# Kernel tuning notes

Measured on AMD Instinct MI355X. Metric: run time of the kernel, lower is better.

## Reference

```python
import jax, jax.numpy as jnp
import numpy as np

B, L, D, H = 2, 2048, 1024, 16
HD = D // H
KW = 4  # conv kernel width


def layernorm(x, g, b, eps=1e-5):
    m = jnp.mean(x, axis=-1, keepdims=True)
    v = jnp.var(x, axis=-1, keepdims=True)
    return (x - m) / jnp.sqrt(v + eps) * g + b


def causal_conv(x, w, b):
    # torch Conv1d(k=4, padding=3, groups=D) then truncate to L => causal depthwise conv
    # out[t] = sum_j w[:, j] * x[t - 3 + j] + b
    xp = jnp.pad(x, ((0, 0), (KW - 1, 0), (0, 0)))
    Lx = x.shape[1]
    out = b
    for j in range(KW):
        out = out + xp[:, j:j + Lx, :] * w[:, j]
    return out


def setup_inputs() -> dict:
    key = jax.random.key(0)
    ks = jax.random.split(key, 16)
    r = lambda i, shape, s=0.02: jax.random.normal(ks[i], shape, jnp.float32) * s
    return dict(
        x=r(0, (B, L, D), 1.0),
        Wqkv=r(1, (D, 3 * D)), Wout=r(2, (D, D)),
        Wgate=r(3, (D, D)), bgate=jnp.zeros((D,), jnp.float32),
        fn_g=jnp.ones((D,), jnp.float32), fn_b=jnp.zeros((D,), jnp.float32),
        dn_g=jnp.ones((D,), jnp.float32), dn_b=jnp.zeros((D,), jnp.float32),
        dWq=r(4, (D, D)), dWk=r(5, (D, D)), dWv=r(6, (D, D)), dWo=r(7, (D, D)),
        Wbeta=r(8, (D, H)), bbeta=jnp.zeros((H,), jnp.float32),
        cq_w=r(9, (D, KW), 0.1), cq_b=jnp.zeros((D,), jnp.float32),
        ck_w=r(10, (D, KW), 0.1), ck_b=jnp.zeros((D,), jnp.float32),
        ln_g=jnp.ones((D,), jnp.float32), ln_b=jnp.zeros((D,), jnp.float32),
    )


def _delta_scan(q, k, v, beta):
    # q,k,v: (B,L,H,HD) ; beta: (B,L,H)
    Bx = q.shape[0]
    S0 = jnp.zeros((Bx, H, HD, HD), q.dtype)
    z0 = jnp.zeros((Bx, H, HD), q.dtype)

    def step(carry, inp):
        S, z = carry
        q_t, k_t, v_t, b_t = inp  # (B,H,HD) x3, (B,H)
        y = jnp.einsum('bhij,bhj->bhi', S, q_t)
        denom = jnp.einsum('bhi,bhi->bh', z, q_t)[..., None] + 1e-6
        y = y / denom
        old = jnp.einsum('bhij,bhj->bhi', S, k_t)
        delta = v_t - old
        S = S + b_t[..., None, None] * jnp.einsum('bhi,bhj->bhij', delta, k_t)
        z = z + b_t[..., None] * k_t
        return (S, z), y

    xs = (jnp.moveaxis(q, 1, 0), jnp.moveaxis(k, 1, 0),
          jnp.moveaxis(v, 1, 0), jnp.moveaxis(beta, 1, 0))
    (S, z), ys = jax.lax.scan(step, (S0, z0), xs)
    return jnp.moveaxis(ys, 0, 1), S, z  # (B,L,H,HD)


def _forward(x, Wqkv, Wout, Wgate, bgate, fn_g, fn_b, dn_g, dn_b,
             dWq, dWk, dWv, dWo, Wbeta, bbeta, cq_w, cq_b, ck_w, ck_b, ln_g, ln_b):
    Bx, Lx, Dx = x.shape
    # ---- flash (full causal, L<=2048 branch) ----
    qkv = (x @ Wqkv).reshape(Bx, Lx, 3, H, HD)
    q = jnp.moveaxis(qkv[:, :, 0], 1, 2)  # (B,H,L,HD)
    k = jnp.moveaxis(qkv[:, :, 1], 1, 2)
    v = jnp.moveaxis(qkv[:, :, 2], 1, 2)
    scale = HD ** -0.5
    scores = jnp.einsum('bhqd,bhkd->bhqk', q, k) * scale
    causal = jnp.tril(jnp.ones((Lx, Lx), bool))
    scores = jnp.where(causal, scores, -jnp.inf)
    attn = jax.nn.softmax(scores, axis=-1)
    flash = jnp.einsum('bhqk,bhkd->bhqd', attn, v)
    flash = jnp.moveaxis(flash, 1, 2).reshape(Bx, Lx, Dx) @ Wout
    flash = layernorm(flash, fn_g, fn_b)
    # ---- delta branch ----
    dq = causal_conv(x @ dWq, cq_w, cq_b).reshape(Bx, Lx, H, HD)
    dk = causal_conv(x @ dWk, ck_w, ck_b).reshape(Bx, Lx, H, HD)
    dv = (x @ dWv).reshape(Bx, Lx, H, HD)
    dk = dk / jnp.maximum(jnp.linalg.norm(dk, axis=-1, keepdims=True), 1e-12)
    beta = jax.nn.sigmoid(x @ Wbeta + bbeta)  # (B,L,H)
    ys, S, z = _delta_scan(dq, dk, dv, beta)
    delta_out = layernorm(ys.reshape(Bx, Lx, Dx) @ dWo, ln_g, ln_b)  # DeltaAttention layer_norm
    delta_out = layernorm(delta_out, dn_g, dn_b)  # hybrid delta_norm
    # ---- gate ----
    gate = jax.nn.sigmoid(x @ Wgate + bgate)
    out = gate * flash + (1.0 - gate) * delta_out
    return out, S, z


def reference(x, Wqkv, Wout, Wgate, bgate, fn_g, fn_b, dn_g, dn_b,
              dWq, dWk, dWv, dWo, Wbeta, bbeta, cq_w, cq_b, ck_w, ck_b, ln_g, ln_b):
    return _forward(x, Wqkv, Wout, Wgate, bgate, fn_g, fn_b, dn_g, dn_b,
                    dWq, dWk, dWv, dWo, Wbeta, bbeta, cq_w, cq_b, ck_w, ck_b, ln_g, ln_b)
```

## Files before the change

kernel.cpp:

```cpp
#include <hip/hip_runtime.h>
#include <hip/hip_bf16.h>

constexpr int B_ = 2, L_ = 2048, D_ = 1024, H_ = 16;

using bf16x8 = __attribute__((ext_vector_type(8))) short;
using f32x4  = __attribute__((ext_vector_type(4))) float;

__device__ __forceinline__ short f2b(float f) {
  union { float f; unsigned int u; } v; v.f = f;
  unsigned int r = (v.u + 0x7FFFu + ((v.u >> 16) & 1u)) >> 16;
  return (short)r;
}
__device__ __forceinline__ float b2f(unsigned short h) {
  union { unsigned int u; float f; } v; v.u = ((unsigned int)h) << 16; return v.f;
}
__device__ __forceinline__ void split2(float x, float y, unsigned int& h, unsigned int& l) {
  unsigned short hx = (unsigned short)f2b(x), hy = (unsigned short)f2b(y);
  h = (unsigned int)hx | ((unsigned int)hy << 16);
  unsigned short lx = (unsigned short)f2b(x - b2f(hx)), ly = (unsigned short)f2b(y - b2f(hy));
  l = (unsigned int)lx | ((unsigned int)ly << 16);
}
__device__ __forceinline__ float dot4(float4 a, float4 b) {
  return a.x * b.x + a.y * b.y + a.z * b.z + a.w * b.w;
}

__global__ __launch_bounds__(256) void tcast(const float* __restrict__ W, short* __restrict__ Wt,
                                             int N, int K) {
  __shared__ float T[64][65];
  int n0 = blockIdx.x * 64, k0 = blockIdx.y * 64;
  int tid = threadIdx.x;
#pragma unroll
  for (int i = 0; i < 16; ++i) {
    int idx = i * 256 + tid;
    int r = idx >> 6, c = idx & 63;
    T[r][c] = W[(size_t)(k0 + r) * N + n0 + c];
  }
  __syncthreads();
#pragma unroll
  for (int i = 0; i < 16; ++i) {
    int idx = i * 256 + tid;
    int rr = idx >> 6, cc = idx & 63;
    Wt[(size_t)(n0 + rr) * K + k0 + cc] = f2b(T[cc][rr]);
  }
}

__global__ __launch_bounds__(256) void tcast2(const float* __restrict__ W1, const float* __restrict__ W2,
                                              short* __restrict__ Wt1, short* __restrict__ Wt2) {
  __shared__ float T[64][65];
  const float* W = blockIdx.z ? W2 : W1;
  short* Wt = blockIdx.z ? Wt2 : Wt1;
  int n0 = blockIdx.x * 64, k0 = blockIdx.y * 64;
  int tid = threadIdx.x;
#pragma unroll
  for (int i = 0; i < 16; ++i) {
    int idx = i * 256 + tid;
    int r = idx >> 6, c = idx & 63;
    T[r][c] = W[(size_t)(k0 + r) * 1024 + n0 + c];
  }
  __syncthreads();
#pragma unroll
  for (int i = 0; i < 16; ++i) {
    int idx = i * 256 + tid;
    int rr = idx >> 6, cc = idx & 63;
    Wt[(size_t)(n0 + rr) * 1024 + k0 + cc] = f2b(T[cc][rr]);
  }
}

__global__ __launch_bounds__(256) void tcast_split2(const float* __restrict__ W1, const float* __restrict__ W2,
                                                    short* __restrict__ Wh1, short* __restrict__ Wl1,
                                                    short* __restrict__ Wh2, short* __restrict__ Wl2) {
  __shared__ float T[64][65];
  const float* W = blockIdx.z ? W2 : W1;
  short* Wh = blockIdx.z ? Wh2 : Wh1;
  short* Wl = blockIdx.z ? Wl2 : Wl1;
  int n0 = blockIdx.x * 64, k0 = blockIdx.y * 64;
  int tid = threadIdx.x;
#pragma unroll
  for (int i = 0; i < 16; ++i) {
    int idx = i * 256 + tid;
    int r = idx >> 6, c = idx & 63;
    T[r][c] = W[(size_t)(k0 + r) * 1024 + n0 + c];
  }
  __syncthreads();
#pragma unroll
  for (int i = 0; i < 16; ++i) {
    int idx = i * 256 + tid;
    int rr = idx >> 6, cc = idx & 63;
    float w = T[cc][rr];
    short h = f2b(w);
    short l = f2b(w - b2f((unsigned short)h));
    size_t o = (size_t)(n0 + rr) * 1024 + k0 + cc;
    Wh[o] = h;
    Wl[o] = l;
  }
}

template <int BN, typename CT>
__device__ __forceinline__ void gemm_bt_body(const float* __restrict__ A, const short* __restrict__ Wt,
                                             CT* __restrict__ C, int N, int K, int bx, int by) {
  constexpr int MT = (BN == 128) ? 4 : 2;
  constexpr int NT = 4;
  __shared__ __align__(16) short As[128 * 32];
  __shared__ __align__(16) short Bs[BN * 32];
  int tid = threadIdx.x;
  int wave = tid >> 6, lane = tid & 63, quad = lane >> 4, l15 = lane & 15;
  int m0 = by * 128, n0 = bx * BN;
  int wm = (BN == 128) ? (wave >> 1) * 64 : wave * 32;
  int wn = (BN == 128) ? (wave & 1) * 64 : 0;
  f32x4 acc[MT][NT];
#pragma unroll
  for (int mt = 0; mt < MT; ++mt)
#pragma unroll
    for (int nt = 0; nt < NT; ++nt) acc[mt][nt] = (f32x4){0.f, 0.f, 0.f, 0.f};

  for (int k0 = 0; k0 < K; k0 += 32) {
    __syncthreads();
#pragma unroll
    for (int i = 0; i < 2; ++i) {
      int chunk = i * 256 + tid;
      int m = chunk >> 2, kc = (chunk & 3) * 8;
      const float* ap = A + (size_t)(m0 + m) * K + k0 + kc;
      float4 a0 = *(const float4*)ap;
      float4 a1 = *(const float4*)(ap + 4);
      __hip_bfloat162 c0 = __float22bfloat162_rn(make_float2(a0.x, a0.y));
      __hip_bfloat162 c1 = __float22bfloat162_rn(make_float2(a0.z, a0.w));
      __hip_bfloat162 c2 = __float22bfloat162_rn(make_float2(a1.x, a1.y));
      __hip_bfloat162 c3 = __float22bfloat162_rn(make_float2(a1.z, a1.w));
      uint4 u;
      u.x = *(unsigned int*)&c0; u.y = *(unsigned int*)&c1;
      u.z = *(unsigned int*)&c2; u.w = *(unsigned int*)&c3;
      *(uint4*)&As[m * 32 + kc] = u;
    }
#pragma unroll
    for (int i = 0; i < BN * 4 / 256; ++i) {
      int chunk = i * 256 + tid;
      int n = chunk >> 2, kc = (chunk & 3) * 8;
      uint4 w = *(const uint4*)(Wt + (size_t)(n0 + n) * K + k0 + kc);
      *(uint4*)&Bs[n * 32 + kc] = w;
    }
    __syncthreads();
    bf16x8 af[MT], bf[NT];
#pragma unroll
    for (int mt = 0; mt < MT; ++mt) af[mt] = *(bf16x8*)&As[(wm + mt * 16 + l15) * 32 + quad * 8];
#pragma unroll
    for (int nt = 0; nt < NT; ++nt) bf[nt] = *(bf16x8*)&Bs[(wn + nt * 16 + l15) * 32 + quad * 8];
#pragma unroll
    for (int mt = 0; mt < MT; ++mt)
#pragma unroll
      for (int nt = 0; nt < NT; ++nt)
        acc[mt][nt] = __builtin_amdgcn_mfma_f32_16x16x32_bf16(af[mt], bf[nt], acc[mt][nt], 0, 0, 0);
  }
#pragma unroll
  for (int mt = 0; mt < MT; ++mt)
#pragma unroll
    for (int nt = 0; nt < NT; ++nt)
#pragma unroll
      for (int r = 0; r < 4; ++r) {
        size_t idx = (size_t)(m0 + wm + mt * 16 + quad * 4 + r) * N + n0 + wn + nt * 16 + l15;
        if constexpr (sizeof(CT) == 2) C[idx] = f2b(acc[mt][nt][r]);
        else C[idx] = acc[mt][nt][r];
      }
}

__global__ __launch_bounds__(256) void gemm_bt_h(const float* __restrict__ A, const short* __restrict__ Wt,
                                                 short* __restrict__ C, int N, int K) {
  gemm_bt_body<128, short>(A, Wt, C, N, K, blockIdx.x, blockIdx.y);
}

__global__ __launch_bounds__(256) void gemm_bt2(const float* __restrict__ A, const short* __restrict__ Wt1,
                                                const short* __restrict__ Wt2, float* __restrict__ C1,
                                                float* __restrict__ C2) {
  gemm_bt_body<64, float>(A, blockIdx.z ? Wt2 : Wt1, blockIdx.z ? C2 : C1, 1024, 1024,
                          blockIdx.x, blockIdx.y);
}

__global__ __launch_bounds__(256) void gemm_bt2_hA(const short* __restrict__ A1, const short* __restrict__ Wt1,
                                                   const short* __restrict__ A2, const short* __restrict__ Wt2,
                                                   float* __restrict__ C1, float* __restrict__ C2) {
  constexpr int K = 1024, N = 1024;
  const short* A = blockIdx.z ? A2 : A1;
  const short* Wt = blockIdx.z ? Wt2 : Wt1;
  float* C = blockIdx.z ? C2 : C1;
  __shared__ __align__(16) short As[128 * 32];
  __shared__ __align__(16) short Bs[64 * 32];
  int tid = threadIdx.x;
  int wave = tid >> 6, lane = tid & 63, quad = lane >> 4, l15 = lane & 15;
  int m0 = blockIdx.y * 128, n0 = blockIdx.x * 64;
  int wm = wave * 32;
  f32x4 acc[2][4];
#pragma unroll
  for (int mt = 0; mt < 2; ++mt)
#pragma unroll
    for (int nt = 0; nt < 4; ++nt) acc[mt][nt] = (f32x4){0.f, 0.f, 0.f, 0.f};
  for (int k0 = 0; k0 < K; k0 += 32) {
    __syncthreads();
#pragma unroll
    for (int i = 0; i < 2; ++i) {
      int chunk = i * 256 + tid;
      int m = chunk >> 2, kc = (chunk & 3) * 8;
      *(uint4*)&As[m * 32 + kc] = *(const uint4*)(A + (size_t)(m0 + m) * K + k0 + kc);
    }
    {
      int n = tid >> 2, kc = (tid & 3) * 8;
      *(uint4*)&Bs[n * 32 + kc] = *(const uint4*)(Wt + (size_t)(n0 + n) * K + k0 + kc);
    }
    __syncthreads();
    bf16x8 af[2], bf[4];
#pragma unroll
    for (int mt = 0; mt < 2; ++mt) af[mt] = *(bf16x8*)&As[(wm + mt * 16 + l15) * 32 + quad * 8];
#pragma unroll
    for (int nt = 0; nt < 4; ++nt) bf[nt] = *(bf16x8*)&Bs[(nt * 16 + l15) * 32 + quad * 8];
#pragma unroll
    for (int mt = 0; mt < 2; ++mt)
#pragma unroll
      for (int nt = 0; nt < 4; ++nt)
        acc[mt][nt] = __builtin_amdgcn_mfma_f32_16x16x32_bf16(af[mt], bf[nt], acc[mt][nt], 0, 0, 0);
  }
#pragma unroll
  for (int mt = 0; mt < 2; ++mt)
#pragma unroll
    for (int nt = 0; nt < 4; ++nt)
#pragma unroll
      for (int r = 0; r < 4; ++r) {
        size_t idx = (size_t)(m0 + wm + mt * 16 + quad * 4 + r) * N + n0 + nt * 16 + l15;
        C[idx] = acc[mt][nt][r];
      }
}

__global__ __launch_bounds__(256) void gemm_bt_split2(const float* __restrict__ A,
                                                      const short* __restrict__ Wh1, const short* __restrict__ Wl1,
                                                      const short* __restrict__ Wh2, const short* __restrict__ Wl2,
                                                      float* __restrict__ C1, float* __restrict__ C2) {
  constexpr int K = 1024, N = 1024;
  const short* Wh = blockIdx.z ? Wh2 : Wh1;
  const short* Wl = blockIdx.z ? Wl2 : Wl1;
  float* C = blockIdx.z ? C2 : C1;
  __shared__ __align__(16) short Ash[128 * 32];
  __shared__ __align__(16) short Asl[128 * 32];
  __shared__ __align__(16) short Bsh[64 * 32];
  __shared__ __align__(16) short Bsl[64 * 32];
  int tid = threadIdx.x;
  int wave = tid >> 6, lane = tid & 63, quad = lane >> 4, l15 = lane & 15;
  int m0 = blockIdx.y * 128, n0 = blockIdx.x * 64;
  int wm = wave * 32;
  f32x4 acc[2][4];
#pragma unroll
  for (int mt = 0; mt < 2; ++mt)
#pragma unroll
    for (int nt = 0; nt < 4; ++nt) acc[mt][nt] = (f32x4){0.f, 0.f, 0.f, 0.f};

  for (int k0 = 0; k0 < K; k0 += 32) {
    __syncthreads();
#pragma unroll
    for (int i = 0; i < 2; ++i) {
      int chunk = i * 256 + tid;
      int m = chunk >> 2, kc = (chunk & 3) * 8;
      const float* ap = A + (size_t)(m0 + m) * K + k0 + kc;
      float4 a0 = *(const float4*)ap;
      float4 a1 = *(const float4*)(ap + 4);
      uint4 uh, ul;
      split2(a0.x, a0.y, uh.x, ul.x);
      split2(a0.z, a0.w, uh.y, ul.y);
      split2(a1.x, a1.y, uh.z, ul.z);
      split2(a1.z, a1.w, uh.w, ul.w);
      *(uint4*)&Ash[m * 32 + kc] = uh;
      *(uint4*)&Asl[m * 32 + kc] = ul;
    }
    {
      int n = tid >> 2, kc = (tid & 3) * 8;
      size_t off = (size_t)(n0 + n) * K + k0 + kc;
      *(uint4*)&Bsh[n * 32 + kc] = *(const uint4*)(Wh + off);
      *(uint4*)&Bsl[n * 32 + kc] = *(const uint4*)(Wl + off);
    }
    __syncthreads();
    bf16x8 ah[2], al[2], bh[4], bl[4];
#pragma unroll
    for (int mt = 0; mt < 2; ++mt) {
      ah[mt] = *(bf16x8*)&Ash[(wm + mt * 16 + l15) * 32 + quad * 8];
      al[mt] = *(bf16x8*)&Asl[(wm + mt * 16 + l15) * 32 + quad * 8];
    }
#pragma unroll
    for (int nt = 0; nt < 4; ++nt) {
      bh[nt] = *(bf16x8*)&Bsh[(nt * 16 + l15) * 32 + quad * 8];
      bl[nt] = *(bf16x8*)&Bsl[(nt * 16 + l15) * 32 + quad * 8];
    }
#pragma unroll
    for (int mt = 0; mt < 2; ++mt)
#pragma unroll
      for (int nt = 0; nt < 4; ++nt) {
        f32x4 a = acc[mt][nt];
        a = __builtin_amdgcn_mfma_f32_16x16x32_bf16(al[mt], bh[nt], a, 0, 0, 0);
        a = __builtin_amdgcn_mfma_f32_16x16x32_bf16(ah[mt], bl[nt], a, 0, 0, 0);
        a = __builtin_amdgcn_mfma_f32_16x16x32_bf16(ah[mt], bh[nt], a, 0, 0, 0);
        acc[mt][nt] = a;
      }
  }
#pragma unroll
  for (int mt = 0; mt < 2; ++mt)
#pragma unroll
    for (int nt = 0; nt < 4; ++nt)
#pragma unroll
      for (int r = 0; r < 4; ++r) {
        size_t idx = (size_t)(m0 + wm + mt * 16 + quad * 4 + r) * N + n0 + nt * 16 + l15;
        C[idx] = acc[mt][nt][r];
      }
}

struct DeltaSmem {
  float MKl[2][32 * 68];
  float BqMl[2][32 * 36];
  float Vl[2][32 * 5];
  float bll[2][32];
  float dnl[2][32];
  float zil[2][64];
  float S0l[4 * 68];
  float Y0l[32 * 5];
  float Rtl[4 * 36];
  float z0l[64];
  float qzl[32];
};
struct AttnSmem {
  short Kl[64 * 64];
  short Vt[64 * 64];
  short Pl[64 * 64];
};

__device__ __forceinline__ void delta_body(char* smraw, int bidx,
                                           const float* __restrict__ dq, const float* __restrict__ dk,
                                           const float* __restrict__ dv, const float* __restrict__ beta,
                                           const float* __restrict__ MK_g, const float* __restrict__ BqM_g,
                                           const float* __restrict__ denB_g, const float* __restrict__ zinc_g,
                                           short* __restrict__ ys_h, float* __restrict__ outS,
                                           float* __restrict__ outZ) {
  DeltaSmem& sm = *reinterpret_cast<DeltaSmem*>(smraw);
  int bh = bidx & 31, grp = bidx >> 5;
  int b = bh >> 4, h = bh & 15;
  int i0 = grp * 4;
  int tid = threadIdx.x;
  int r = tid >> 3, j8 = (tid & 7) * 8;
  int js = tid & 7;
  size_t kqbase = (size_t)(b * L_) * 1024 + h * 64;

  for (int e = tid; e < 4 * 68; e += 256) sm.S0l[e] = 0.f;
  if (tid < 64) sm.z0l[tid] = 0.f;

  float4 kAc, kBc, qAc, qBc, kAn, kBn, qAn, qBn;
  float4 mA, mB, bqA, bqB;
  bqA = bqB = make_float4(0.f, 0.f, 0.f, 0.f);
  float vr = 0.f, blr = 0.f, dnb = 0.f, zi = 0.f;

#define KQLOAD(CN, KA, KB, QA, QB) { \
    size_t rb_ = kqbase + (size_t)((CN) * 32 + r) * 1024 + j8; \
    KA = ((const float4*)(dk + rb_))[0]; KB = ((const float4*)(dk + rb_))[1]; \
    QA = ((const float4*)(dq + rb_))[0]; QB = ((const float4*)(dq + rb_))[1]; \
  }
#define AUXLOAD(CN) { \
    size_t cb_ = (size_t)(bh * 64 + (CN)); \
    const float* mkp_ = MK_g + (cb_ * 32 + r) * 64 + j8; \
    mA = ((const float4*)mkp_)[0]; mB = ((const float4*)mkp_)[1]; \
    if (tid < 128) { \
      const float* bqp_ = BqM_g + cb_ * 1024 + (tid >> 2) * 32 + (tid & 3) * 8; \
      bqA = ((const float4*)bqp_)[0]; bqB = ((const float4*)bqp_)[1]; \
      vr = dv[(size_t)(b * L_ + (CN) * 32 + (tid >> 2)) * 1024 + h * 64 + i0 + (tid & 3)]; \
    } \
    if (tid < 32) { blr = beta[(size_t)(b * L_ + (CN) * 32 + tid) * 16 + h]; dnb = denB_g[cb_ * 32 + tid]; } \
    if (tid < 64) zi = zinc_g[cb_ * 64 + tid]; \
  }
#define AUXSTORE(NX) { \
    *(float4*)&sm.MKl[NX][r * 68 + j8] = mA; *(float4*)&sm.MKl[NX][r * 68 + j8 + 4] = mB; \
    if (tid < 128) { \
      int t_ = tid >> 2, s8_ = (tid & 3) * 8; \
      *(float4*)&sm.BqMl[NX][t_ * 36 + s8_] = bqA; \
      *(float4*)&sm.BqMl[NX][t_ * 36 + s8_ + 4] = bqB; \
      sm.Vl[NX][t_ * 5 + (tid & 3)] = vr; \
    } \
    if (tid < 32) { sm.bll[NX][tid] = blr; sm.dnl[NX][tid] = dnb; } \
    if (tid < 64) sm.zil[NX][tid] = zi; \
  }

  KQLOAD(0, kAc, kBc, qAc, qBc);
  AUXLOAD(0);
  AUXSTORE(0);
  __syncthreads();

  for (int c = 0; c < 64; ++c) {
    int cur = c & 1, nxt = cur ^ 1;
    int cn = (c + 1 < 64) ? c + 1 : 63;
    KQLOAD(cn, kAn, kBn, qAn, qBn);
    AUXLOAD(cn);
    {
      float aK[4], aY[4];
#pragma unroll
      for (int i = 0; i < 4; ++i) {
        float4 s0 = *(float4*)&sm.S0l[i * 68 + j8];
        float4 s1 = *(float4*)&sm.S0l[i * 68 + j8 + 4];
        aK[i] = dot4(kAc, s0) + dot4(kBc, s1);
        aY[i] = dot4(qAc, s0) + dot4(qBc, s1);
      }
      float4 z0 = *(float4*)&sm.z0l[j8];
      float4 z1 = *(float4*)&sm.z0l[j8 + 4];
      float aZ = dot4(qAc, z0) + dot4(qBc, z1);
#pragma unroll
      for (int off = 1; off <= 4; off <<= 1) {
#pragma unroll
        for (int i = 0; i < 4; ++i) {
          aK[i] += __shfl_xor(aK[i], off);
          aY[i] += __shfl_xor(aY[i], off);
        }
        aZ += __shfl_xor(aZ, off);
      }
      if (js == 0) {
        float be = sm.bll[cur][r];
#pragma unroll
        for (int i = 0; i < 4; ++i) {
          sm.Rtl[i * 36 + r] = be * (sm.Vl[cur][r * 5 + i] - aK[i]);
          sm.Y0l[r * 5 + i] = aY[i];
        }
        sm.qzl[r] = aZ;
      }
    }
    __syncthreads();
    if (tid < 128) {
      int i2 = tid >> 5;
      int j2 = (tid & 31) * 2;
      float a0 = sm.S0l[i2 * 68 + j2];
      float a1 = sm.S0l[i2 * 68 + j2 + 1];
#pragma unroll
      for (int s4i = 0; s4i < 8; ++s4i) {
        float4 rt = *(float4*)&sm.Rtl[i2 * 36 + s4i * 4];
        float2 m0 = *(float2*)&sm.MKl[cur][(s4i * 4 + 0) * 68 + j2];
        float2 m1 = *(float2*)&sm.MKl[cur][(s4i * 4 + 1) * 68 + j2];
        float2 m2 = *(float2*)&sm.MKl[cur][(s4i * 4 + 2) * 68 + j2];
        float2 m3 = *(float2*)&sm.MKl[cur][(s4i * 4 + 3) * 68 + j2];
        a0 += rt.x * m0.x + rt.y * m1.x + rt.z * m2.x + rt.w * m3.x;
        a1 += rt.x * m0.y + rt.y * m1.y + rt.z * m2.y + rt.w * m3.y;
      }
      sm.S0l[i2 * 68 + j2] = a0;
      sm.S0l[i2 * 68 + j2 + 1] = a1;
      if (tid < 64) sm.z0l[tid] += sm.zil[cur][tid];
    } else {
      int t = (tid >> 2) & 31;
      int i = tid & 3;
      float acc = sm.Y0l[t * 5 + i];
#pragma unroll
      for (int s4i = 0; s4i < 8; ++s4i)
        acc += dot4(*(float4*)&sm.BqMl[cur][t * 36 + s4i * 4], *(float4*)&sm.Rtl[i * 36 + s4i * 4]);
      float y = acc / (sm.qzl[t] + sm.dnl[cur][t] + 1e-6f);
      ys_h[(size_t)(b * L_ + c * 32 + t) * 1024 + h * 64 + i0 + i] = f2b(y);
    }
    AUXSTORE(nxt);
    kAc = kAn; kBc = kBn; qAc = qAn; qBc = qBn;
    __syncthreads();
  }
#undef KQLOAD
#undef AUXLOAD
#undef AUXSTORE
  {
    int i = tid >> 6, j = tid & 63;
    outS[((size_t)(bh * 64) + i0 + i) * 64 + j] = sm.S0l[i * 68 + j];
  }
  if (grp == 0 && tid < 64) outZ[bh * 64 + tid] = sm.z0l[tid];
}

__device__ __forceinline__ void attn_body(char* smraw, int idx, const short* __restrict__ qkv,
                                          short* __restrict__ outp_h) {
  AttnSmem& sm = *reinterpret_cast<AttnSmem*>(smraw);
  int qb = 31 - (idx & 31), h = (idx >> 5) & 15, b = idx >> 9;
  int tid = threadIdx.x;
  int wave = tid >> 6, lane = tid & 63;
  int quad = lane >> 4, l15 = lane & 15;
  int qrow = qb * 64 + wave * 16 + l15;
  bf16x8 qf[2];
  {
    const short* qbase = qkv + (size_t)(b * L_ + qrow) * 3072 + h * 64;
#pragma unroll
    for (int s = 0; s < 2; ++s) qf[s] = *(const bf16x8*)(qbase + s * 32 + quad * 8);
  }
  f32x4 Of[4];
  float mrow[4], lrow[4], alpha[4];
#pragma unroll
  for (int dt = 0; dt < 4; ++dt) Of[dt] = (f32x4){0.f, 0.f, 0.f, 0.f};
#pragma unroll
  for (int r = 0; r < 4; ++r) { mrow[r] = -1e30f; lrow[r] = 0.f; }

  for (int kt = 0; kt <= qb; ++kt) {
    __syncthreads();
#pragma unroll
    for (int it = 0; it < 2; ++it) {
      int e8 = tid + it * 256;
      int key = e8 >> 3, g = e8 & 7;
      const short* src = qkv + ((size_t)((b * L_ + kt * 64 + key) * 3) + 1) * 1024 + h * 64 + g * 8;
      *(bf16x8*)&sm.Kl[key * 64 + ((g ^ (key & 7)) << 3)] = *(const bf16x8*)src;
    }
    {
      int key4 = tid >> 4;
      int d4 = tid & 15;
      const short* vsrc = qkv + ((size_t)((b * L_ + kt * 64 + key4 * 4) * 3) + 2) * 1024 + h * 64 + d4 * 4;
      short4 v0 = *(const short4*)vsrc;
      short4 v1 = *(const short4*)(vsrc + 3072);
      short4 v2 = *(const short4*)(vsrc + 6144);
      short4 v3 = *(const short4*)(vsrc + 9216);
      short vr0[4] = {v0.x, v0.y, v0.z, v0.w};
      short vr1[4] = {v1.x, v1.y, v1.z, v1.w};
      short vr2[4] = {v2.x, v2.y, v2.z, v2.w};
      short vr3[4] = {v3.x, v3.y, v3.z, v3.w};
      int kg = key4 >> 1, k7b = (key4 & 1) * 4;
#pragma unroll
      for (int jj = 0; jj < 4; ++jj) {
        int d = d4 * 4 + jj;
        short4 sv;
        sv.x = vr0[jj]; sv.y = vr1[jj]; sv.z = vr2[jj]; sv.w = vr3[jj];
        *(short4*)&sm.Vt[d * 64 + ((kg ^ (d & 7)) << 3) + k7b] = sv;
      }
    }
    __syncthreads();
    f32x4 sc[4];
#pragma unroll
    for (int nt = 0; nt < 4; ++nt) sc[nt] = (f32x4){0.f, 0.f, 0.f, 0.f};
#pragma unroll
    for (int s = 0; s < 2; ++s) {
#pragma unroll
      for (int nt = 0; nt < 4; ++nt) {
        int key = nt * 16 + l15;
        bf16x8 kf = *(bf16x8*)&sm.Kl[key * 64 + (((4 * s + quad) ^ (key & 7)) << 3)];
        sc[nt] = __builtin_amdgcn_mfma_f32_16x16x32_bf16(qf[s], kf, sc[nt], 0, 0, 0);
      }
    }
    bool diag = (kt == qb);
#pragma unroll
    for (int r = 0; r < 4; ++r) {
      float sv[4];
#pragma unroll
      for (int nt = 0; nt < 4; ++nt) {
        float v = sc[nt][r] * 0.125f;
        if (diag && (nt * 16 + l15 > wave * 16 + quad * 4 + r)) v = -1e30f;
        sv[nt] = v;
      }
      float mx = fmaxf(fmaxf(sv[0], sv[1]), fmaxf(sv[2], sv[3]));
      mx = fmaxf(mx, __shfl_xor(mx, 1));
      mx = fmaxf(mx, __shfl_xor(mx, 2));
      mx = fmaxf(mx, __shfl_xor(mx, 4));
      mx = fmaxf(mx, __shfl_xor(mx, 8));
      float mnew = fmaxf(mrow[r], mx);
      float al = __expf(mrow[r] - mnew);
      mrow[r] = mnew;
      alpha[r] = al;
      int prow = wave * 16 + quad * 4 + r;
      int r7 = prow & 7;
      float ps = 0.f;
#pragma unroll
      for (int nt = 0; nt < 4; ++nt) {
        float p = __expf(sv[nt] - mnew);
        ps += p;
        sm.Pl[prow * 64 + ((((nt << 1) + (l15 >> 3)) ^ r7) << 3) + (l15 & 7)] = f2b(p);
      }
      ps += __shfl_xor(ps, 1);
      ps += __shfl_xor(ps, 2);
      ps += __shfl_xor(ps, 4);
      ps += __shfl_xor(ps, 8);
      lrow[r] = lrow[r] * al + ps;
    }
#pragma unroll
    for (int dt = 0; dt < 4; ++dt)
#pragma unroll
      for (int r = 0; r < 4; ++r) Of[dt][r] *= alpha[r];
#pragma unroll
    for (int s = 0; s < 2; ++s) {
      bf16x8 pf = *(bf16x8*)&sm.Pl[(wave * 16 + l15) * 64 + (((4 * s + quad) ^ (l15 & 7)) << 3)];
#pragma unroll
      for (int dt = 0; dt < 4; ++dt) {
        int d = dt * 16 + l15;
        bf16x8 vf = *(bf16x8*)&sm.Vt[d * 64 + (((4 * s + quad) ^ (d & 7)) << 3)];
        Of[dt] = __builtin_amdgcn_mfma_f32_16x16x32_bf16(pf, vf, Of[dt], 0, 0, 0);
      }
    }
  }
#pragma unroll
  for (int r = 0; r < 4; ++r) alpha[r] = 1.f / lrow[r];
  int orow = qb * 64 + wave * 16 + quad * 4;
#pragma unroll
  for (int dt = 0; dt < 4; ++dt)
#pragma unroll
    for (int r = 0; r < 4; ++r)
      outp_h[(size_t)(b * L_ + orow + r) * 1024 + h * 64 + dt * 16 + l15] = f2b(Of[dt][r] * alpha[r]);
}

__global__ __launch_bounds__(256) void attn_delta_fused(
    const short* __restrict__ qkv, short* __restrict__ attnO_h,
    const float* __restrict__ dq, const float* __restrict__ dk,
    const float* __restrict__ dv, const float* __restrict__ beta,
    const float* __restrict__ MK_g, const float* __restrict__ BqM_g,
    const float* __restrict__ denB_g, const float* __restrict__ zinc_g,
    short* __restrict__ ys_h, float* __restrict__ outS, float* __restrict__ outZ) {
  __shared__ __align__(16) char smem[sizeof(DeltaSmem)];
  static_assert(sizeof(DeltaSmem) >= sizeof(AttnSmem), "overlay");
  if (blockIdx.x < 512)
    delta_body(smem, blockIdx.x, dq, dk, dv, beta, MK_g, BqM_g, denB_g, zinc_g, ys_h, outS, outZ);
  else
    attn_body(smem, blockIdx.x - 512, qkv, attnO_h);
}

__global__ __launch_bounds__(256) void ln2mix_f(const float* __restrict__ X,
                                                const float* __restrict__ g1, const float* __restrict__ b1,
                                                const float* __restrict__ g2, const float* __restrict__ b2,
                                                const float* __restrict__ gpre, const float* __restrict__ bgate,
                                                const float* __restrict__ foraw,
                                                const float* __restrict__ fng, const float* __restrict__ fnb,
                                                float* __restrict__ outp) {
  int row = blockIdx.x, tid = threadIdx.x;
  const float* xr = X + (size_t)row * D_;
  const float* fr = foraw + (size_t)row * D_;
  __shared__ float rs[4], rss[4], frs[4], frss[4];
  float v[4], f[4];
  float s = 0.f, ss = 0.f, fs = 0.f, fss = 0.f;
#pragma unroll
  for (int i = 0; i < 4; ++i) {
    v[i] = xr[tid + i * 256]; s += v[i]; ss += v[i] * v[i];
    f[i] = fr[tid + i * 256]; fs += f[i]; fss += f[i] * f[i];
  }
#pragma unroll
  for (int off = 32; off; off >>= 1) {
    s += __shfl_xor(s, off); ss += __shfl_xor(ss, off);
    fs += __shfl_xor(fs, off); fss += __shfl_xor(fss, off);
  }
  if ((tid & 63) == 0) { rs[tid >> 6] = s; rss[tid >> 6] = ss; frs[tid >> 6] = fs; frss[tid >> 6] = fss; }
  __syncthreads();
  float S = rs[0] + rs[1] + rs[2] + rs[3];
  float SS = rss[0] + rss[1] + rss[2] + rss[3];
  float FS = frs[0] + frs[1] + frs[2] + frs[3];
  float FSS = frss[0] + frss[1] + frss[2] + frss[3];
  float mean = S * (1.f / 1024.f);
  float var = SS * (1.f / 1024.f) - mean * mean;
  float inv = rsqrtf(var + 1e-5f);
  float fmean = FS * (1.f / 1024.f);
  float fvar = FSS * (1.f / 1024.f) - fmean * fmean;
  float finv = rsqrtf(fvar + 1e-5f);
  s = 0.f; ss = 0.f;
#pragma unroll
  for (int i = 0; i < 4; ++i) {
    int c = tid + i * 256;
    v[i] = (v[i] - mean) * inv * g1[c] + b1[c];
    s += v[i]; ss += v[i] * v[i];
  }
#pragma unroll
  for (int off = 32; off; off >>= 1) { s += __shfl_xor(s, off); ss += __shfl_xor(ss, off); }
  __syncthreads();
  if ((tid & 63) == 0) { rs[tid >> 6] = s; rss[tid >> 6] = ss; }
  __syncthreads();
  S = rs[0] + rs[1] + rs[2] + rs[3];
  SS = rss[0] + rss[1] + rss[2] + rss[3];
  mean = S * (1.f / 1024.f);
  var = SS * (1.f / 1024.f) - mean * mean;
  inv = rsqrtf(var + 1e-5f);
#pragma unroll
  for (int i = 0; i < 4; ++i) {
    int c = tid + i * 256;
    size_t idx = (size_t)row * D_ + c;
    float w = (v[i] - mean) * inv * g2[c] + b2[c];
    float fl = (f[i] - fmean) * finv * fng[c] + fnb[c];
    float gg = 1.f / (1.f + __expf(-(gpre[idx] + bgate[c])));
    outp[idx] = gg * fl + (1.f - gg) * w;
  }
}

__global__ __launch_bounds__(256) void convnorm_kernel(const float* __restrict__ qin, const float* __restrict__ kin,
                                                       const float* __restrict__ qw, const float* __restrict__ qb,
                                                       const float* __restrict__ kw, const float* __restrict__ kb,
                                                       float* __restrict__ qout, float* __restrict__ kout) {
  int path = blockIdx.y;
  int row = blockIdx.x * 4 + (threadIdx.x >> 6);
  int lane = threadIdx.x & 63;
  int bl = row >> 4, h = row & 15;
  int t = bl & (L_ - 1);
  int d = h * 64 + lane;
  size_t idx = (size_t)bl * D_ + d;
  const float* xin = path ? kin : qin;
  const float* w = path ? kw : qw;
  const float* bias = path ? kb : qb;
  float acc = bias[d];
#pragma unroll
  for (int j = 0; j < 4; ++j) {
    int tt = t - 3 + j;
    if (tt >= 0) acc += w[d * 4 + j] * xin[idx + (size_t)(j - 3) * D_];
  }
  if (path) {
    float n2 = acc * acc;
#pragma unroll
    for (int off = 32; off; off >>= 1) n2 += __shfl_xor(n2, off);
    acc = acc / fmaxf(sqrtf(n2), 1e-12f);
    kout[idx] = acc;
  } else {
    qout[idx] = acc;
  }
}

__global__ __launch_bounds__(256) void beta_kernel(const float* __restrict__ xf, const float* __restrict__ Wb,
                                                   const float* __restrict__ bb, float* __restrict__ beta) {
  int row = blockIdx.x, tid = threadIdx.x;
  int h = tid & 15, seg = tid >> 4;
  const float* xr = xf + (size_t)row * D_ + seg * 64;
  const float* wp = Wb + (seg * 64) * H_ + h;
  float p = 0.f;
  for (int k = 0; k < 64; ++k) p += xr[k] * wp[k * H_];
  __shared__ float red[16][17];
  red[seg][h] = p;
  __syncthreads();
  if (tid < 16) {
    float s = bb[tid];
#pragma unroll
    for (int s2 = 0; s2 < 16; ++s2) s += red[s2][tid];
    beta[(size_t)row * H_ + tid] = 1.f / (1.f + __expf(-s));
  }
}

__global__ __launch_bounds__(256) void prep_kernel(const float* __restrict__ dq, const float* __restrict__ dk,
                                                   const float* __restrict__ beta,
                                                   float* __restrict__ MK_g, float* __restrict__ BqM_g,
                                                   float* __restrict__ denB_g, float* __restrict__ zinc_g) {
  __shared__ __align__(16) float Kl[32 * 68];
  __shared__ __align__(16) float Ql[32 * 68];
  __shared__ __align__(16) float Ml[32 * 36];
  __shared__ __align__(16) float Xl[32 * 36];
  __shared__ __align__(16) float Bql[32 * 36];
  __shared__ __align__(16) float bl[32];
  int c = blockIdx.x, bh = blockIdx.y;
  int b = bh >> 4, h = bh & 15;
  int t0 = c * 32;
  int tid = threadIdx.x;
#pragma unroll
  for (int rep = 0; rep < 2; ++rep) {
    int id = tid * 2 + rep;
    int r = id >> 4, j4 = id & 15;
    size_t gi = (size_t)(b * L_ + t0 + r) * 1024 + h * 64 + j4 * 4;
    *(float4*)&Kl[r * 68 + j4 * 4] = *(const float4*)&dk[gi];
    *(float4*)&Ql[r * 68 + j4 * 4] = *(const float4*)&dq[gi];
  }
  if (tid < 32) bl[tid] = beta[(size_t)(b * L_ + t0 + tid) * 16 + h];
  __syncthreads();
  int t = tid >> 3, s0 = (tid & 7) * 4;
  float accA[4] = {0.f, 0.f, 0.f, 0.f}, accB[4] = {0.f, 0.f, 0.f, 0.f};
#pragma unroll
  for (int k4 = 0; k4 < 16; ++k4) {
    float4 kt = *(float4*)&Kl[t * 68 + k4 * 4];
    float4 qt = *(float4*)&Ql[t * 68 + k4 * 4];
#pragma unroll
    for (int j = 0; j < 4; ++j) {
      float4 ks = *(float4*)&Kl[(s0 + j) * 68 + k4 * 4];
      accA[j] += dot4(kt, ks);
      accB[j] += dot4(qt, ks);
    }
  }
#pragma unroll
  for (int j = 0; j < 4; ++j) {
    int s = s0 + j;
    Ml[t * 36 + s] = (s < t) ? bl[t] * accA[j] : ((s == t) ? 1.f : 0.f);
    Bql[t * 36 + s] = (s < t) ? accB[j] : 0.f;
  }
  __syncthreads();
  if (tid < 32) {
    int col = tid;
    float xr[32];
#pragma unroll
    for (int tt = 0; tt < 32; ++tt) {
      float x = (tt == col) ? 1.f : 0.f;
#pragma unroll
      for (int s = 0; s < tt; ++s) x -= Ml[tt * 36 + s] * xr[s];
      xr[tt] = x;
      Xl[tt * 36 + col] = x;
    }
  }
  __syncthreads();
  size_t cb = (size_t)(bh * 64 + c);
  {
    int s = tid >> 3, j8 = (tid & 7) * 8;
    float4 m0 = make_float4(0.f, 0.f, 0.f, 0.f);
    float4 m1 = make_float4(0.f, 0.f, 0.f, 0.f);
#pragma unroll
    for (int t2 = 0; t2 < 32; ++t2) {
      float xv = Xl[t2 * 36 + s];
      float4 k0 = *(float4*)&Kl[t2 * 68 + j8];
      float4 k1 = *(float4*)&Kl[t2 * 68 + j8 + 4];
      m0.x += xv * k0.x; m0.y += xv * k0.y; m0.z += xv * k0.z; m0.w += xv * k0.w;
      m1.x += xv * k1.x; m1.y += xv * k1.y; m1.z += xv * k1.z; m1.w += xv * k1.w;
    }
    float* mkp = MK_g + (cb * 32 + s) * 64 + j8;
    *(float4*)mkp = m0;
    *(float4*)(mkp + 4) = m1;
  }
  {
    int tt = tid >> 3, s4 = (tid & 7) * 4;
    float4 acc = make_float4(0.f, 0.f, 0.f, 0.f);
#pragma unroll
    for (int u4 = 0; u4 < 8; ++u4) {
      float4 bq = *(float4*)&Bql[tt * 36 + u4 * 4];
      float4 x0 = *(float4*)&Xl[(u4 * 4 + 0) * 36 + s4];
      float4 x1 = *(float4*)&Xl[(u4 * 4 + 1) * 36 + s4];
      float4 x2 = *(float4*)&Xl[(u4 * 4 + 2) * 36 + s4];
      float4 x3 = *(float4*)&Xl[(u4 * 4 + 3) * 36 + s4];
      acc.x += bq.x * x0.x + bq.y * x1.x + bq.z * x2.x + bq.w * x3.x;
      acc.y += bq.x * x0.y + bq.y * x1.y + bq.z * x2.y + bq.w * x3.y;
      acc.z += bq.x * x0.z + bq.y * x1.z + bq.z * x2.z + bq.w * x3.z;
      acc.w += bq.x * x0.w + bq.y * x1.w + bq.z * x2.w + bq.w * x3.w;
    }
    *(float4*)&BqM_g[cb * 1024 + tt * 32 + s4] = acc;
  }
  if (tid < 32) {
    float a = 0.f;
#pragma unroll
    for (int s4i = 0; s4i < 8; ++s4i)
      a += dot4(*(float4*)&Bql[tid * 36 + s4i * 4], *(float4*)&bl[s4i * 4]);
    denB_g[cb * 32 + tid] = a;
  }
  if (tid >= 64 && tid < 128) {
    int j = tid - 64;
    float a = 0.f;
#pragma unroll
    for (int s = 0; s < 32; ++s) a += bl[s] * Kl[s * 68 + j];
    zinc_g[cb * 64 + j] = a;
  }
}

extern "C" void kernel_launch(void* const* d_in, const int* in_sizes, int n_in,
                              void* d_out, int out_size, void* d_ws, size_t ws_size,
                              hipStream_t stream) {
  const float* x     = (const float*)d_in[0];
  const float* Wqkv  = (const float*)d_in[1];
  const float* Wout  = (const float*)d_in[2];
  const float* Wgate = (const float*)d_in[3];
  const float* bgate = (const float*)d_in[4];
  const float* fn_g  = (const float*)d_in[5];
  const float* fn_b  = (const float*)d_in[6];
  const float* dn_g  = (const float*)d_in[7];
  const float* dn_b  = (const float*)d_in[8];
  const float* dWq   = (const float*)d_in[9];
  const float* dWk   = (const float*)d_in[10];
  const float* dWv   = (const float*)d_in[11];
  const float* dWo   = (const float*)d_in[12];
  const float* Wbeta = (const float*)d_in[13];
  const float* bbeta = (const float*)d_in[14];
  const float* cq_w  = (const float*)d_in[15];
  const float* cq_b  = (const float*)d_in[16];
  const float* ck_w  = (const float*)d_in[17];
  const float* ck_b  = (const float*)d_in[18];
  const float* ln_g  = (const float*)d_in[19];
  const float* ln_b  = (const float*)d_in[20];

  float* ws = (float*)d_ws;
  float* dqc    = ws;
  float* dkc    = ws + 4194304;
  float* dv     = ws + 8388608;
  float* gpre   = ws + 12582912;
  float* MK_g   = ws + 16777216;
  float* BqM_g  = ws + 20971520;
  float* denB_g = ws + 23068672;
  float* zinc_g = ws + 23134208;
  float* betab  = ws + 23265280;
  short* qkvh   = (short*)(ws + 23330816);
  short* Wqh = (short*)(ws + 16777216);
  short* Wql = (short*)(ws + 17301504);
  short* Wkh = (short*)(ws + 17825792);
  short* Wkl = (short*)(ws + 18350080);
  float* dqp = ws + 18874368;
  float* dkp = ws + 23330816;
  short* Wvt = (short*)(ws + 16777216);
  short* wtg = (short*)(ws + 17301504);
  short* Wqkvt = (short*)(ws + 16777216);
  short* Woutt = (short*)(ws + 4194304);
  short* Wot   = (short*)(ws + 4718592);
  float* fo    = ws + 16777216;
  float* do1   = ws + 8388608;

  float* out  = (float*)d_out;
  float* outS = out + 4194304;
  float* outZ = out + 4325376;
  short* ysb_h   = (short*)out;
  short* attnO_h = (short*)(out + 2097152);

  tcast_split2<<<dim3(16, 16, 2), 256, 0, stream>>>(dWq, dWk, Wqh, Wql, Wkh, Wkl);
  gemm_bt_split2<<<dim3(16, 32, 2), 256, 0, stream>>>(x, Wqh, Wql, Wkh, Wkl, dqp, dkp);
  convnorm_kernel<<<dim3(16384, 2), 256, 0, stream>>>(dqp, dkp, cq_w, cq_b, ck_w, ck_b, dqc, dkc);
  beta_kernel<<<4096, 256, 0, stream>>>(x, Wbeta, bbeta, betab);
  tcast2<<<dim3(16, 16, 2), 256, 0, stream>>>(dWv, Wgate, Wvt, wtg);
  gemm_bt2<<<dim3(16, 32, 2), 256, 0, stream>>>(x, Wvt, wtg, dv, gpre);
  tcast<<<dim3(48, 16), 256, 0, stream>>>(Wqkv, Wqkvt, 3072, 1024);
  gemm_bt_h<<<dim3(24, 32), 256, 0, stream>>>(x, Wqkvt, qkvh, 3072, 1024);
  prep_kernel<<<dim3(64, 32), 256, 0, stream>>>(dqc, dkc, betab, MK_g, BqM_g, denB_g, zinc_g);
  attn_delta_fused<<<1536, 256, 0, stream>>>(qkvh, attnO_h, dqc, dkc, dv, betab,
                                             MK_g, BqM_g, denB_g, zinc_g, ysb_h, outS, outZ);
  tcast2<<<dim3(16, 16, 2), 256, 0, stream>>>(Wout, dWo, Woutt, Wot);
  gemm_bt2_hA<<<dim3(16, 32, 2), 256, 0, stream>>>(attnO_h, Woutt, ysb_h, Wot, fo, do1);
  ln2mix_f<<<4096, 256, 0, stream>>>(do1, ln_g, ln_b, dn_g, dn_b, gpre, bgate, fo, fn_g, fn_b, out);
}
```

Baseline: 701.7 us.

## Merge weight casts and independent GEMMs into combined launches; read BqM from global

All five weight transpose/cast jobs are merged into one tcast_all launch. The QKV GEMM, the dv/gate GEMMs and the beta projection are merged into one heterogeneous gemm3_beta launch that shares a shared-memory buffer. The intent is to cut launch count and fill the GPU better with independent work. In the delta kernel, the BqM tile is no longer staged into shared memory; it is read straight from global memory, which shrinks shared memory use but adds uncached-style global reads in the output loop. The workspace layout is reshuffled so the buffers do not alias across the new launch order.

```diff
diff --git a/kernel.cpp b/kernel.cpp
--- a/kernel.cpp
+++ b/kernel.cpp
@@ -24,23 +24,48 @@
   return a.x * b.x + a.y * b.y + a.z * b.z + a.w * b.w;
 }
 
-__global__ __launch_bounds__(256) void tcast(const float* __restrict__ W, short* __restrict__ Wt,
-                                             int N, int K) {
+__global__ __launch_bounds__(256) void tcast_all(const float* __restrict__ Wqkv,
+                                                 const float* __restrict__ dWq, const float* __restrict__ dWk,
+                                                 const float* __restrict__ dWv, const float* __restrict__ Wgate,
+                                                 short* __restrict__ Wqkvt,
+                                                 short* __restrict__ Wqh, short* __restrict__ Wql,
+                                                 short* __restrict__ Wkh, short* __restrict__ Wkl,
+                                                 short* __restrict__ Wvt, short* __restrict__ wtg) {
   __shared__ float T[64][65];
-  int n0 = blockIdx.x * 64, k0 = blockIdx.y * 64;
+  int idx = blockIdx.x;
+  const float* W;
+  short* O1;
+  short* O2 = nullptr;
+  int N, bx, by;
+  if (idx < 768) {
+    W = Wqkv; O1 = Wqkvt; N = 3072; bx = idx % 48; by = idx / 48;
+  } else if (idx < 1280) {
+    int rem = idx - 768; int z = rem >> 8;
+    W = z ? dWk : dWq; O1 = z ? Wkh : Wqh; O2 = z ? Wkl : Wql; N = 1024;
+    bx = rem & 15; by = (rem >> 4) & 15;
+  } else {
+    int rem = idx - 1280; int z = rem >> 8;
+    W = z ? Wgate : dWv; O1 = z ? wtg : Wvt; N = 1024;
+    bx = rem & 15; by = (rem >> 4) & 15;
+  }
+  int n0 = bx * 64, k0 = by * 64;
   int tid = threadIdx.x;
 #pragma unroll
   for (int i = 0; i < 16; ++i) {
-    int idx = i * 256 + tid;
-    int r = idx >> 6, c = idx & 63;
+    int id2 = i * 256 + tid;
+    int r = id2 >> 6, c = id2 & 63;
     T[r][c] = W[(size_t)(k0 + r) * N + n0 + c];
   }
   __syncthreads();
 #pragma unroll
   for (int i = 0; i < 16; ++i) {
-    int idx = i * 256 + tid;
-    int rr = idx >> 6, cc = idx & 63;
-    Wt[(size_t)(n0 + rr) * K + k0 + cc] = f2b(T[cc][rr]);
+    int id2 = i * 256 + tid;
+    int rr = id2 >> 6, cc = id2 & 63;
+    float w = T[cc][rr];
+    short h = f2b(w);
+    size_t o = (size_t)(n0 + rr) * 1024 + k0 + cc;
+    O1[o] = h;
+    if (O2) O2[o] = f2b(w - b2f((unsigned short)h));
   }
 }
 
@@ -66,42 +91,14 @@
   }
 }
 
-__global__ __launch_bounds__(256) void tcast_split2(const float* __restrict__ W1, const float* __restrict__ W2,
-                                                    short* __restrict__ Wh1, short* __restrict__ Wl1,
-                                                    short* __restrict__ Wh2, short* __restrict__ Wl2) {
-  __shared__ float T[64][65];
-  const float* W = blockIdx.z ? W2 : W1;
-  short* Wh = blockIdx.z ? Wh2 : Wh1;
-  short* Wl = blockIdx.z ? Wl2 : Wl1;
-  int n0 = blockIdx.x * 64, k0 = blockIdx.y * 64;
-  int tid = threadIdx.x;
-#pragma unroll
-  for (int i = 0; i < 16; ++i) {
-    int idx = i * 256 + tid;
-    int r = idx >> 6, c = idx & 63;
-    T[r][c] = W[(size_t)(k0 + r) * 1024 + n0 + c];
-  }
-  __syncthreads();
-#pragma unroll
-  for (int i = 0; i < 16; ++i) {
-    int idx = i * 256 + tid;
-    int rr = idx >> 6, cc = idx & 63;
-    float w = T[cc][rr];
-    short h = f2b(w);
-    short l = f2b(w - b2f((unsigned short)h));
-    size_t o = (size_t)(n0 + rr) * 1024 + k0 + cc;
-    Wh[o] = h;
-    Wl[o] = l;
-  }
-}
-
 template <int BN, typename CT>
-__device__ __forceinline__ void gemm_bt_body(const float* __restrict__ A, const short* __restrict__ Wt,
-                                             CT* __restrict__ C, int N, int K, int bx, int by) {
+__device__ __forceinline__ void gemm_bt_body(char* smraw, const float* __restrict__ A,
+                                             const short* __restrict__ Wt, CT* __restrict__ C,
+                                             int N, int K, int bx, int by) {
   constexpr int MT = (BN == 128) ? 4 : 2;
   constexpr int NT = 4;
-  __shared__ __align__(16) short As[128 * 32];
-  __shared__ __align__(16) short Bs[BN * 32];
+  short* As = (short*)smraw;
+  short* Bs = (short*)(smraw + 8192);
   int tid = threadIdx.x;
   int wave = tid >> 6, lane = tid & 63, quad = lane >> 4, l15 = lane & 15;
   int m0 = by * 128, n0 = bx * BN;
@@ -162,16 +159,43 @@
       }
 }
 
-__global__ __launch_bounds__(256) void gemm_bt_h(const float* __restrict__ A, const short* __restrict__ Wt,
-                                                 short* __restrict__ C, int N, int K) {
-  gemm_bt_body<128, short>(A, Wt, C, N, K, blockIdx.x, blockIdx.y);
-}
-
-__global__ __launch_bounds__(256) void gemm_bt2(const float* __restrict__ A, const short* __restrict__ Wt1,
-                                                const short* __restrict__ Wt2, float* __restrict__ C1,
-                                                float* __restrict__ C2) {
-  gemm_bt_body<64, float>(A, blockIdx.z ? Wt2 : Wt1, blockIdx.z ? C2 : C1, 1024, 1024,
-                          blockIdx.x, blockIdx.y);
+__device__ __forceinline__ void beta_body(char* smraw, const float* __restrict__ xf,
+                                          const float* __restrict__ Wb, const float* __restrict__ bb,
+                                          float* __restrict__ beta, int row) {
+  float (*red)[17] = (float(*)[17])smraw;
+  int tid = threadIdx.x;
+  int h = tid & 15, seg = tid >> 4;
+  const float* xr = xf + (size_t)row * D_ + seg * 64;
+  const float* wp = Wb + (seg * 64) * H_ + h;
+  float p = 0.f;
+  for (int k = 0; k < 64; ++k) p += xr[k] * wp[k * H_];
+  red[seg][h] = p;
+  __syncthreads();
+  if (tid < 16) {
+    float s = bb[tid];
+#pragma unroll
+    for (int s2 = 0; s2 < 16; ++s2) s += red[s2][tid];
+    beta[(size_t)row * H_ + tid] = 1.f / (1.f + __expf(-s));
+  }
+}
+
+__global__ __launch_bounds__(256) void gemm3_beta(const float* __restrict__ x,
+                                                  const short* __restrict__ Wqkvt, short* __restrict__ qkvh,
+                                                  const short* __restrict__ Wvt, const short* __restrict__ wtg,
+                                                  float* __restrict__ dv, float* __restrict__ gpre,
+                                                  const float* __restrict__ Wb, const float* __restrict__ bb,
+                                                  float* __restrict__ betab) {
+  __shared__ __align__(16) char smem[16384];
+  int idx = blockIdx.x;
+  if (idx < 768) {
+    gemm_bt_body<128, short>(smem, x, Wqkvt, qkvh, 3072, 1024, idx % 24, idx / 24);
+  } else if (idx < 1792) {
+    int rem = idx - 768;
+    int z = rem >> 9;
+    gemm_bt_body<64, float>(smem, x, z ? wtg : Wvt, z ? gpre : dv, 1024, 1024, rem & 15, (rem >> 4) & 31);
+  } else {
+    beta_body(smem, x, Wb, bb, betab, idx - 1792);
+  }
 }
 
 __global__ __launch_bounds__(256) void gemm_bt2_hA(const short* __restrict__ A1, const short* __restrict__ Wt1,
@@ -308,7 +332,6 @@
 
 struct DeltaSmem {
   float MKl[2][32 * 68];
-  float BqMl[2][32 * 36];
   float Vl[2][32 * 5];
   float bll[2][32];
   float dnl[2][32];
@@ -324,6 +347,7 @@
   short Vt[64 * 64];
   short Pl[64 * 64];
 };
+constexpr size_t SMEM_MAX = sizeof(DeltaSmem) > sizeof(AttnSmem) ? sizeof(DeltaSmem) : sizeof(AttnSmem);
 
 __device__ __forceinline__ void delta_body(char* smraw, int bidx,
                                            const float* __restrict__ dq, const float* __restrict__ dk,
@@ -345,8 +369,7 @@
   if (tid < 64) sm.z0l[tid] = 0.f;
 
   float4 kAc, kBc, qAc, qBc, kAn, kBn, qAn, qBn;
-  float4 mA, mB, bqA, bqB;
-  bqA = bqB = make_float4(0.f, 0.f, 0.f, 0.f);
+  float4 mA, mB;
   float vr = 0.f, blr = 0.f, dnb = 0.f, zi = 0.f;
 
 #define KQLOAD(CN, KA, KB, QA, QB) { \
@@ -359,8 +382,6 @@
     const float* mkp_ = MK_g + (cb_ * 32 + r) * 64 + j8; \
     mA = ((const float4*)mkp_)[0]; mB = ((const float4*)mkp_)[1]; \
     if (tid < 128) { \
-      const float* bqp_ = BqM_g + cb_ * 1024 + (tid >> 2) * 32 + (tid & 3) * 8; \
-      bqA = ((const float4*)bqp_)[0]; bqB = ((const float4*)bqp_)[1]; \
       vr = dv[(size_t)(b * L_ + (CN) * 32 + (tid >> 2)) * 1024 + h * 64 + i0 + (tid & 3)]; \
     } \
     if (tid < 32) { blr = beta[(size_t)(b * L_ + (CN) * 32 + tid) * 16 + h]; dnb = denB_g[cb_ * 32 + tid]; } \
@@ -368,12 +389,7 @@
   }
 #define AUXSTORE(NX) { \
     *(float4*)&sm.MKl[NX][r * 68 + j8] = mA; *(float4*)&sm.MKl[NX][r * 68 + j8 + 4] = mB; \
-    if (tid < 128) { \
-      int t_ = tid >> 2, s8_ = (tid & 3) * 8; \
-      *(float4*)&sm.BqMl[NX][t_ * 36 + s8_] = bqA; \
-      *(float4*)&sm.BqMl[NX][t_ * 36 + s8_ + 4] = bqB; \
-      sm.Vl[NX][t_ * 5 + (tid & 3)] = vr; \
-    } \
+    if (tid < 128) sm.Vl[NX][(tid >> 2) * 5 + (tid & 3)] = vr; \
     if (tid < 32) { sm.bll[NX][tid] = blr; sm.dnl[NX][tid] = dnb; } \
     if (tid < 64) sm.zil[NX][tid] = zi; \
   }
@@ -439,12 +455,14 @@
       sm.S0l[i2 * 68 + j2 + 1] = a1;
       if (tid < 64) sm.z0l[tid] += sm.zil[cur][tid];
     } else {
+      size_t cbc = (size_t)(bh * 64 + c);
       int t = (tid >> 2) & 31;
       int i = tid & 3;
+      const float* bqr = BqM_g + cbc * 1024 + t * 32;
       float acc = sm.Y0l[t * 5 + i];
 #pragma unroll
       for (int s4i = 0; s4i < 8; ++s4i)
-        acc += dot4(*(float4*)&sm.BqMl[cur][t * 36 + s4i * 4], *(float4*)&sm.Rtl[i * 36 + s4i * 4]);
+        acc += dot4(*(const float4*)(bqr + s4i * 4), *(float4*)&sm.Rtl[i * 36 + s4i * 4]);
       float y = acc / (sm.qzl[t] + sm.dnl[cur][t] + 1e-6f);
       ys_h[(size_t)(b * L_ + c * 32 + t) * 1024 + h * 64 + i0 + i] = f2b(y);
     }
@@ -592,8 +610,7 @@
     const float* __restrict__ MK_g, const float* __restrict__ BqM_g,
     const float* __restrict__ denB_g, const float* __restrict__ zinc_g,
     short* __restrict__ ys_h, float* __restrict__ outS, float* __restrict__ outZ) {
-  __shared__ __align__(16) char smem[sizeof(DeltaSmem)];
-  static_assert(sizeof(DeltaSmem) >= sizeof(AttnSmem), "overlay");
+  __shared__ __align__(16) char smem[SMEM_MAX];
   if (blockIdx.x < 512)
     delta_body(smem, blockIdx.x, dq, dk, dv, beta, MK_g, BqM_g, denB_g, zinc_g, ys_h, outS, outZ);
   else
@@ -691,25 +708,6 @@
     kout[idx] = acc;
   } else {
     qout[idx] = acc;
-  }
-}
-
-__global__ __launch_bounds__(256) void beta_kernel(const float* __restrict__ xf, const float* __restrict__ Wb,
-                                                   const float* __restrict__ bb, float* __restrict__ beta) {
-  int row = blockIdx.x, tid = threadIdx.x;
-  int h = tid & 15, seg = tid >> 4;
-  const float* xr = xf + (size_t)row * D_ + seg * 64;
-  const float* wp = Wb + (seg * 64) * H_ + h;
-  float p = 0.f;
-  for (int k = 0; k < 64; ++k) p += xr[k] * wp[k * H_];
-  __shared__ float red[16][17];
-  red[seg][h] = p;
-  __syncthreads();
-  if (tid < 16) {
-    float s = bb[tid];
-#pragma unroll
-    for (int s2 = 0; s2 < 16; ++s2) s += red[s2][tid];
-    beta[(size_t)row * H_ + tid] = 1.f / (1.f + __expf(-s));
   }
 }
 
@@ -850,25 +848,25 @@
   float* dkc    = ws + 4194304;
   float* dv     = ws + 8388608;
   float* gpre   = ws + 12582912;
-  float* MK_g   = ws + 16777216;
-  float* BqM_g  = ws + 20971520;
-  float* denB_g = ws + 23068672;
-  float* zinc_g = ws + 23134208;
-  float* betab  = ws + 23265280;
-  short* qkvh   = (short*)(ws + 23330816);
-  short* Wqh = (short*)(ws + 16777216);
-  short* Wql = (short*)(ws + 17301504);
-  short* Wkh = (short*)(ws + 17825792);
-  short* Wkl = (short*)(ws + 18350080);
-  float* dqp = ws + 18874368;
-  float* dkp = ws + 23330816;
-  short* Wvt = (short*)(ws + 16777216);
-  short* wtg = (short*)(ws + 17301504);
-  short* Wqkvt = (short*)(ws + 16777216);
-  short* Woutt = (short*)(ws + 4194304);
-  short* Wot   = (short*)(ws + 4718592);
-  float* fo    = ws + 16777216;
-  float* do1   = ws + 8388608;
+  float* betab  = ws + 16777216;
+  float* denB_g = ws + 16842752;
+  float* zinc_g = ws + 16908288;
+  float* MK_g   = ws + 17039360;
+  short* Wqh    = (short*)(ws + 16777216);
+  short* Wql    = (short*)(ws + 17301504);
+  short* Wkh    = (short*)(ws + 17825792);
+  short* Wkl    = (short*)(ws + 18350080);
+  short* Wvt    = (short*)(ws + 18874368);
+  short* wtg    = (short*)(ws + 19398656);
+  short* Wqkvt  = (short*)(ws + 19922944);
+  float* dqp    = ws + 21495808;
+  float* dkp    = ws + 25690112;
+  short* qkvh   = (short*)(ws + 21495808);
+  float* BqM_g  = ws + 27787264;
+  short* Woutt  = (short*)ws;
+  short* Wot    = (short*)(ws + 524288);
+  float* do1    = ws + 4194304;
+  float* fo     = ws + 8388608;
 
   float* out  = (float*)d_out;
   float* outS = out + 4194304;
@@ -876,14 +874,10 @@
   short* ysb_h   = (short*)out;
   short* attnO_h = (short*)(out + 2097152);
 
-  tcast_split2<<<dim3(16, 16, 2), 256, 0, stream>>>(dWq, dWk, Wqh, Wql, Wkh, Wkl);
+  tcast_all<<<1792, 256, 0, stream>>>(Wqkv, dWq, dWk, dWv, Wgate, Wqkvt, Wqh, Wql, Wkh, Wkl, Wvt, wtg);
   gemm_bt_split2<<<dim3(16, 32, 2), 256, 0, stream>>>(x, Wqh, Wql, Wkh, Wkl, dqp, dkp);
   convnorm_kernel<<<dim3(16384, 2), 256, 0, stream>>>(dqp, dkp, cq_w, cq_b, ck_w, ck_b, dqc, dkc);
-  beta_kernel<<<4096, 256, 0, stream>>>(x, Wbeta, bbeta, betab);
-  tcast2<<<dim3(16, 16, 2), 256, 0, stream>>>(dWv, Wgate, Wvt, wtg);
-  gemm_bt2<<<dim3(16, 32, 2), 256, 0, stream>>>(x, Wvt, wtg, dv, gpre);
-  tcast<<<dim3(48, 16), 256, 0, stream>>>(Wqkv, Wqkvt, 3072, 1024);
-  gemm_bt_h<<<dim3(24, 32), 256, 0, stream>>>(x, Wqkvt, qkvh, 3072, 1024);
+  gemm3_beta<<<5888, 256, 0, stream>>>(x, Wqkvt, qkvh, Wvt, wtg, dv, gpre, Wbeta, bbeta, betab);
   prep_kernel<<<dim3(64, 32), 256, 0, stream>>>(dqc, dkc, betab, MK_g, BqM_g, denB_g, zinc_g);
   attn_delta_fused<<<1536, 256, 0, stream>>>(qkvh, attnO_h, dqc, dkc, dv, betab,
                                              MK_g, BqM_g, denB_g, zinc_g, ysb_h, outS, outZ);
```

Result: no change. 698.5 us (-0.5%).
